# Kernel tuning notes

Hardware: AMD Instinct MI355X
Metric: run time of the kernel (lower is better)

## Reference

```python
import jax, jax.numpy as jnp
import numpy as np

N, D = 16384, 256

def setup_inputs() -> dict:
    key = jax.random.key(0)
    kA, kx, kW = jax.random.split(key, 3)
    A = jax.random.normal(kA, (N, N), dtype=jnp.float32)
    x = jax.random.normal(kx, (N, D), dtype=jnp.float32)
    # nn.Linear(input_dim, 1): weight (1, D) -> stored transposed as (D, 1), bias (1,)
    W = jax.random.normal(kW, (D, 1), dtype=jnp.float32) / np.sqrt(D)
    b = jnp.zeros((1,), dtype=jnp.float32)
    return {"A": A, "x": x, "W": W, "b": b, "k": 8192}

def reference(A, x, W, b, k):
    # proj_scores = sigmoid(Linear(x)).squeeze()  -> (N,)
    scores = jax.nn.sigmoid(x @ W + b)[:, 0]
    # top-k node selection
    vs, idxs = jax.lax.top_k(scores, k)          # (k,), (k,)
    # gather + scale node features
    x_pooled = x[idxs] * vs[:, None]             # (k, D)
    # elementwise square of adjacency, then row/col gather
    A2 = A * A                                   # (N, N)
    A_pooled = A2[idxs][:, idxs]                 # (k, k)
    return A_pooled, x_pooled, idxs
```

## Files before the change

### kernel.cpp

```cpp
#include <hip/hip_runtime.h>
#include <stdint.h>

#define N_NODES 16384
#define DIM     256
#define KSEL    8192

__device__ __forceinline__ float eigen_pexp_f32(float _x)
{
    float x = fminf(fmaxf(_x, -88.0f), 88.0f);
    float m = floorf(__fmaf_rn(x, 1.44269504088896341f, 0.5f));
    float r = __fmaf_rn(m, -0.693359375f, x);
    r = __fmaf_rn(m, 2.12194440e-4f, r);
    float r2 = __fmul_rn(r, r);
    float y = 1.9875691500e-4f;
    y = __fmaf_rn(y, r, 1.3981999507e-3f);
    y = __fmaf_rn(y, r, 8.3334519073e-3f);
    y = __fmaf_rn(y, r, 4.1665795894e-2f);
    y = __fmaf_rn(y, r, 1.6666665459e-1f);
    y = __fmaf_rn(y, r, 5.0000001201e-1f);
    y = __fmaf_rn(y, r2, r);
    y = __fadd_rn(y, 1.0f);
    return ldexpf(y, (int)m);
}

__global__ __launch_bounds__(256) void score_kernel(
    const float* __restrict__ x, const float* __restrict__ W,
    const float* __restrict__ b, float* __restrict__ scores,
    unsigned long long* __restrict__ keys, int* __restrict__ ranks)
{
    const int tid = blockIdx.x * 256 + threadIdx.x;
    const int row = tid >> 3;
    const int l   = tid & 7;

    const float* xr = x + (size_t)row * DIM;
    float a = 0.0f;
    #pragma unroll 8
    for (int it = 0; it < DIM / 8; ++it)
        a = __fmaf_rn(xr[it * 8 + l], W[it * 8 + l], a);

    const float s   = __fadd_rn(a, __shfl_xor(a, 4, 64));
    const float t   = __fadd_rn(s, __shfl_xor(s, 2, 64));
    const float dot = __fadd_rn(t, __shfl_xor(t, 1, 64));

    if (l == 0) {
        const float z = __fadd_rn(dot, b[0]);
        const float e = eigen_pexp_f32(-z);
        const float sc = __fdiv_rn(1.0f, __fadd_rn(1.0f, e));
        scores[row] = sc;
        keys[row] = ((unsigned long long)__float_as_uint(sc) << 32)
                  | (unsigned long long)(0xFFFFFFFFu - (unsigned)row);
        ranks[row] = 0;
    }
}

__global__ __launch_bounds__(256) void rank_kernel(
    const unsigned long long* __restrict__ keys, int* __restrict__ ranks)
{
    __shared__ ulonglong2 sk2[1024];
    const int j0 = blockIdx.y * 2048;
    for (int t = threadIdx.x; t < 1024; t += 256)
        sk2[t] = reinterpret_cast<const ulonglong2*>(keys)[j0 / 2 + t];
    __syncthreads();

    const int i = blockIdx.x * 256 + threadIdx.x;
    const unsigned long long ki = keys[i];
    int cnt = 0;
    #pragma unroll 8
    for (int j = 0; j < 1024; ++j) {
        const ulonglong2 k2 = sk2[j];
        cnt += (k2.x > ki) ? 1 : 0;
        cnt += (k2.y > ki) ? 1 : 0;
    }
    if (cnt) atomicAdd(&ranks[i], cnt);
}

__global__ __launch_bounds__(256) void scatter_kernel(
    const int* __restrict__ ranks, const float* __restrict__ scores,
    int* __restrict__ idxs, float* __restrict__ vs, float* __restrict__ out_idx)
{
    const int i = blockIdx.x * 256 + threadIdx.x;
    const int r = ranks[i];
    if (r < KSEL) {
        idxs[r]    = i;
        vs[r]      = scores[i];
        out_idx[r] = (float)i;
    }
}

__global__ __launch_bounds__(256) void xpool_kernel(
    const float* __restrict__ x, const int* __restrict__ idxs,
    const float* __restrict__ vs, float* __restrict__ outx)
{
    const int wave = (blockIdx.x * 256 + threadIdx.x) >> 6;
    const int lane = threadIdx.x & 63;
    const int row  = idxs[wave];
    const float v  = vs[wave];
    const float4 xv = *reinterpret_cast<const float4*>(x + (size_t)row * DIM + lane * 4);
    float4 o;
    o.x = xv.x * v; o.y = xv.y * v; o.z = xv.z * v; o.w = xv.w * v;
    *reinterpret_cast<float4*>(outx + (size_t)wave * DIM + lane * 4) = o;
}

__global__ __launch_bounds__(256) void apool_kernel(
    const float* __restrict__ A, const int* __restrict__ idxs,
    float* __restrict__ outA)
{
    __shared__ float row[N_NODES];
    const int r    = blockIdx.x;
    const int src  = idxs[r];
    const int wid  = threadIdx.x >> 6;
    const int lane = threadIdx.x & 63;
    const float* arow = A + (size_t)src * N_NODES;

    #pragma unroll
    for (int c = 0; c < 16; ++c) {
        const int chunk = wid * 16 + c;
        const float* gsrc = arow + chunk * 256 + lane * 4;
        float* ldst = &row[chunk * 256];
        __builtin_amdgcn_global_load_lds(
            (const __attribute__((address_space(1))) void*)gsrc,
            (__attribute__((address_space(3))) void*)ldst,
            16, 0, 0);
    }
    __syncthreads();

    float* orow = outA + (size_t)r * KSEL;
    #pragma unroll
    for (int it = 0; it < KSEL / (256 * 4); ++it) {
        const int q = it * 256 + threadIdx.x;
        const int c = q * 4;
        const int4 id4 = *reinterpret_cast<const int4*>(idxs + c);
        float4 o;
        o.x = row[id4.x]; o.y = row[id4.y]; o.z = row[id4.z]; o.w = row[id4.w];
        o.x *= o.x; o.y *= o.y; o.z *= o.z; o.w *= o.w;
        *reinterpret_cast<float4*>(orow + c) = o;
    }
}

extern "C" void kernel_launch(void* const* d_in, const int* in_sizes, int n_in,
                              void* d_out, int out_size, void* d_ws, size_t ws_size,
                              hipStream_t stream)
{
    const float* A = (const float*)d_in[0];
    const float* x = (const float*)d_in[1];
    const float* W = (const float*)d_in[2];
    const float* b = (const float*)d_in[3];
    (void)in_sizes; (void)n_in; (void)out_size; (void)ws_size;

    char* ws = (char*)d_ws;
    unsigned long long* keys = (unsigned long long*)(ws);
    int*    ranks  = (int*)   (ws + 131072);
    float*  scores = (float*) (ws + 196608);
    int*    idxs   = (int*)   (ws + 262144);
    float*  vs     = (float*) (ws + 294912);

    float* outA = (float*)d_out;
    float* outX = outA + (size_t)KSEL * KSEL;
    float* outI = outX + (size_t)KSEL * DIM;

    score_kernel<<<N_NODES * 8 / 256, 256, 0, stream>>>(x, W, b, scores, keys, ranks);
    dim3 rgrid(N_NODES / 256, 8);
    rank_kernel<<<rgrid, 256, 0, stream>>>(keys, ranks);
    scatter_kernel<<<N_NODES / 256, 256, 0, stream>>>(ranks, scores, idxs, vs, outI);
    xpool_kernel<<<KSEL / 4, 256, 0, stream>>>(x, idxs, vs, outX);
    apool_kernel<<<KSEL, 256, 0, stream>>>(A, idxs, outA);
}
```

Measured before the change: 188.8 us.

## Gather only selected columns of A via sorted selection and permutation

Adds a compaction kernel that builds the ascending list of selected node indices and their positions, plus a kernel that maps top-k order to sorted positions. The A pooling kernel now loads only the selected columns of each source row into LDS with 4-byte global-to-LDS loads, then reads them back through the permutation. This halves the LDS footprint and the nominal bytes fetched per row, in exchange for two extra small launches, one of them a single-block serial scan, and narrower scattered loads.

After: 221.9 us. +17.5%, slower.

```diff
diff --git a/kernel.cpp b/kernel.cpp
--- a/kernel.cpp
+++ b/kernel.cpp
@@ -87,6 +87,38 @@
     }
 }
 
+__global__ __launch_bounds__(256) void compact_kernel(
+    const int* __restrict__ ranks, int* __restrict__ pos,
+    int* __restrict__ sorted_sel)
+{
+    __shared__ int csum[256];
+    const int tid = threadIdx.x;
+    int cnt = 0;
+    for (int j = 0; j < 64; ++j)
+        cnt += (ranks[tid * 64 + j] < KSEL) ? 1 : 0;
+    csum[tid] = cnt;
+    __syncthreads();
+    for (int off = 1; off < 256; off <<= 1) {
+        const int v = (tid >= off) ? csum[tid - off] : 0;
+        __syncthreads();
+        csum[tid] += v;
+        __syncthreads();
+    }
+    int base = csum[tid] - cnt;
+    for (int j = 0; j < 64; ++j) {
+        const int i = tid * 64 + j;
+        if (ranks[i] < KSEL) { sorted_sel[base] = i; pos[i] = base; ++base; }
+    }
+}
+
+__global__ __launch_bounds__(256) void perm_kernel(
+    const int* __restrict__ idxs, const int* __restrict__ pos,
+    int* __restrict__ perm)
+{
+    const int c = blockIdx.x * 256 + threadIdx.x;
+    perm[c] = pos[idxs[c]];
+}
+
 __global__ __launch_bounds__(256) void xpool_kernel(
     const float* __restrict__ x, const int* __restrict__ idxs,
     const float* __restrict__ vs, float* __restrict__ outx)
@@ -103,37 +135,41 @@
 
 __global__ __launch_bounds__(256) void apool_kernel(
     const float* __restrict__ A, const int* __restrict__ idxs,
+    const int* __restrict__ sorted_sel, const int* __restrict__ perm,
     float* __restrict__ outA)
 {
-    __shared__ float row[N_NODES];
+    __shared__ float st[KSEL];
     const int r    = blockIdx.x;
     const int src  = idxs[r];
     const int wid  = threadIdx.x >> 6;
     const int lane = threadIdx.x & 63;
     const float* arow = A + (size_t)src * N_NODES;
 
+    int cols[32];
     #pragma unroll
-    for (int c = 0; c < 16; ++c) {
-        const int chunk = wid * 16 + c;
-        const float* gsrc = arow + chunk * 256 + lane * 4;
-        float* ldst = &row[chunk * 256];
+    for (int c = 0; c < 32; ++c)
+        cols[c] = sorted_sel[wid * 2048 + c * 64 + lane];
+
+    #pragma unroll
+    for (int c = 0; c < 32; ++c) {
+        const float* gsrc = arow + cols[c];
+        float* ldst = &st[wid * 2048 + c * 64];
         __builtin_amdgcn_global_load_lds(
             (const __attribute__((address_space(1))) void*)gsrc,
             (__attribute__((address_space(3))) void*)ldst,
-            16, 0, 0);
+            4, 0, 0);
     }
     __syncthreads();
 
     float* orow = outA + (size_t)r * KSEL;
     #pragma unroll
-    for (int it = 0; it < KSEL / (256 * 4); ++it) {
+    for (int it = 0; it < 8; ++it) {
         const int q = it * 256 + threadIdx.x;
-        const int c = q * 4;
-        const int4 id4 = *reinterpret_cast<const int4*>(idxs + c);
+        const int4 p4 = reinterpret_cast<const int4*>(perm)[q];
         float4 o;
-        o.x = row[id4.x]; o.y = row[id4.y]; o.z = row[id4.z]; o.w = row[id4.w];
+        o.x = st[p4.x]; o.y = st[p4.y]; o.z = st[p4.z]; o.w = st[p4.w];
         o.x *= o.x; o.y *= o.y; o.z *= o.z; o.w *= o.w;
-        *reinterpret_cast<float4*>(orow + c) = o;
+        reinterpret_cast<float4*>(orow)[q] = o;
     }
 }
 
@@ -153,6 +189,9 @@
     float*  scores = (float*) (ws + 196608);
     int*    idxs   = (int*)   (ws + 262144);
     float*  vs     = (float*) (ws + 294912);
+    int*    pos    = (int*)   (ws + 327680);
+    int*    ssel   = (int*)   (ws + 393216);
+    int*    perm   = (int*)   (ws + 425984);
 
     float* outA = (float*)d_out;
     float* outX = outA + (size_t)KSEL * KSEL;
@@ -162,6 +201,8 @@
     dim3 rgrid(N_NODES / 256, 8);
     rank_kernel<<<rgrid, 256, 0, stream>>>(keys, ranks);
     scatter_kernel<<<N_NODES / 256, 256, 0, stream>>>(ranks, scores, idxs, vs, outI);
+    compact_kernel<<<1, 256, 0, stream>>>(ranks, pos, ssel);
+    perm_kernel<<<KSEL / 256, 256, 0, stream>>>(idxs, pos, perm);
     xpool_kernel<<<KSEL / 4, 256, 0, stream>>>(x, idxs, vs, outX);
-    apool_kernel<<<KSEL, 256, 0, stream>>>(A, idxs, outA);
-}
+    apool_kernel<<<KSEL, 256, 0, stream>>>(A, idxs, ssel, perm, outA);
+}
```

## Make apool kernel persistent with double-buffered LDS row prefetch

Applied to the files above, without the earlier changes.

The A-pooling kernel now runs 512 persistent blocks of 512 threads. Each block processes 16 rows and double-buffers them in LDS (128KB), issuing the global-to-LDS load for the next selected row while it gathers and squares the current one. The goal is to overlap the HBM row fetch with the LDS gather and output store, instead of relying on many short-lived blocks. In exchange, only one block fits per CU because of the LDS use, and the grid shrinks to 512 blocks, which lowers occupancy and latency hiding.

Result: slower. 199.8 us (+5.8%).

```diff
diff --git a/kernel.cpp b/kernel.cpp
--- a/kernel.cpp
+++ b/kernel.cpp
@@ -101,40 +101,53 @@
     *reinterpret_cast<float4*>(outx + (size_t)wave * DIM + lane * 4) = o;
 }
 
-__global__ __launch_bounds__(256) void apool_kernel(
+__global__ __launch_bounds__(512) void apool_kernel(
     const float* __restrict__ A, const int* __restrict__ idxs,
     float* __restrict__ outA)
 {
-    __shared__ float row[N_NODES];
-    const int r    = blockIdx.x;
-    const int src  = idxs[r];
+    __shared__ float buf[2][N_NODES];
     const int wid  = threadIdx.x >> 6;
     const int lane = threadIdx.x & 63;
-    const float* arow = A + (size_t)src * N_NODES;
 
-    #pragma unroll
-    for (int c = 0; c < 16; ++c) {
-        const int chunk = wid * 16 + c;
-        const float* gsrc = arow + chunk * 256 + lane * 4;
-        float* ldst = &row[chunk * 256];
-        __builtin_amdgcn_global_load_lds(
-            (const __attribute__((address_space(1))) void*)gsrc,
-            (__attribute__((address_space(3))) void*)ldst,
-            16, 0, 0);
+    #define STAGE(slot, r)                                                   \
+        do {                                                                 \
+            const int   _src  = idxs[r];                                     \
+            const float* _arow = A + (size_t)_src * N_NODES;                 \
+            _Pragma("unroll")                                                \
+            for (int _c = 0; _c < 8; ++_c) {                                 \
+                const int _chunk = wid * 8 + _c;                             \
+                const float* _gsrc = _arow + _chunk * 256 + lane * 4;        \
+                float* _ldst = &buf[slot][_chunk * 256];                     \
+                __builtin_amdgcn_global_load_lds(                            \
+                    (const __attribute__((address_space(1))) void*)_gsrc,    \
+                    (__attribute__((address_space(3))) void*)_ldst,          \
+                    16, 0, 0);                                               \
+            }                                                                \
+        } while (0)
+
+    int cur = 0;
+    STAGE(0, (int)blockIdx.x);
+    for (int t = 0; t < 16; ++t) {
+        __syncthreads();
+        if (t + 1 < 16) {
+            const int rn = (t + 1) * 512 + blockIdx.x;
+            STAGE(cur ^ 1, rn);
+        }
+        const int r = t * 512 + blockIdx.x;
+        float* orow = outA + (size_t)r * KSEL;
+        #pragma unroll
+        for (int it = 0; it < 4; ++it) {
+            const int q = it * 512 + threadIdx.x;
+            const int4 id4 = reinterpret_cast<const int4*>(idxs)[q];
+            float4 o;
+            o.x = buf[cur][id4.x]; o.y = buf[cur][id4.y];
+            o.z = buf[cur][id4.z]; o.w = buf[cur][id4.w];
+            o.x *= o.x; o.y *= o.y; o.z *= o.z; o.w *= o.w;
+            reinterpret_cast<float4*>(orow)[q] = o;
+        }
+        cur ^= 1;
     }
-    __syncthreads();
-
-    float* orow = outA + (size_t)r * KSEL;
-    #pragma unroll
-    for (int it = 0; it < KSEL / (256 * 4); ++it) {
-        const int q = it * 256 + threadIdx.x;
-        const int c = q * 4;
-        const int4 id4 = *reinterpret_cast<const int4*>(idxs + c);
-        float4 o;
-        o.x = row[id4.x]; o.y = row[id4.y]; o.z = row[id4.z]; o.w = row[id4.w];
-        o.x *= o.x; o.y *= o.y; o.z *= o.z; o.w *= o.w;
-        *reinterpret_cast<float4*>(orow + c) = o;
-    }
+    #undef STAGE
 }
 
 extern "C" void kernel_launch(void* const* d_in, const int* in_sizes, int n_in,
@@ -163,5 +176,5 @@
     rank_kernel<<<rgrid, 256, 0, stream>>>(keys, ranks);
     scatter_kernel<<<N_NODES / 256, 256, 0, stream>>>(ranks, scores, idxs, vs, outI);
     xpool_kernel<<<KSEL / 4, 256, 0, stream>>>(x, idxs, vs, outX);
-    apool_kernel<<<KSEL, 256, 0, stream>>>(A, idxs, outA);
+    apool_kernel<<<512, 512, 0, stream>>>(A, idxs, outA);
 }
```
